# Kernel tuning notes

Measured on AMD Instinct MI355X. Metric: run time of the kernel, lower is better.

## Reference

```python
import jax, jax.numpy as jnp
import numpy as np

EPS = 1e-5  # BatchNorm1d default eps


def _proj_bn(x, W, gamma, beta, mean, var):
    # Conv1d(kernel=1, bias=False) == channel matmul, then inference BatchNorm1d.
    y = jnp.einsum('oc,bcn->bon', W, x)  # (B, C_out, N)
    scale = gamma / jnp.sqrt(var + EPS)  # (C_out,)
    shift = beta - mean * scale
    return y * scale[:, None] + shift[:, None]


def setup_inputs() -> dict:
    key = jax.random.key(0)
    ks = jax.random.split(key, 8)
    B, C, N = 8, 512, 2048
    inp = {
        'input': jax.random.normal(ks[0], (B, C, N), dtype=jnp.float32),
        'Wq': jax.random.normal(ks[1], (C, C), dtype=jnp.float32) * (1.0 / np.sqrt(C)),
        'gq': jnp.ones((C,), jnp.float32),
        'bq': jnp.zeros((C,), jnp.float32),
        'mq': jax.random.normal(ks[2], (C,), dtype=jnp.float32) * 0.1,
        'vq': jax.random.uniform(ks[3], (C,), dtype=jnp.float32) + 0.5,
        'Wk': jax.random.normal(ks[4], (C, C), dtype=jnp.float32) * (1.0 / np.sqrt(C)),
        'gk': jnp.ones((C,), jnp.float32),
        'bk': jnp.zeros((C,), jnp.float32),
        'mk': jax.random.normal(ks[5], (C,), dtype=jnp.float32) * 0.1,
        'vk': jax.random.uniform(ks[6], (C,), dtype=jnp.float32) + 0.5,
        'Wv': jax.random.normal(ks[7], (C, C), dtype=jnp.float32) * (1.0 / np.sqrt(C)),
        'gv': jnp.ones((C,), jnp.float32),
        'bv': jnp.zeros((C,), jnp.float32),
        'mv': jax.random.normal(jax.random.fold_in(key, 100), (C,), dtype=jnp.float32) * 0.1,
        'vv': jax.random.uniform(jax.random.fold_in(key, 101), (C,), dtype=jnp.float32) + 0.5,
    }
    return inp


def reference(input, Wq, gq, bq, mq, vq, Wk, gk, bk, mk, vk, Wv, gv, bv, mv, vv):
    q = _proj_bn(input, Wq, gq, bq, mq, vq)  # (B, C, N)
    k = _proj_bn(input, Wk, gk, bk, mk, vk)
    v = _proj_bn(input, Wv, gv, bv, mv, vv)
    # w[b, i, j] = sum_c q[b, c, i] * k[b, c, j]
    w = jnp.einsum('bci,bcj->bij', q, k)
    a = jax.nn.softmax(w, axis=-1)  # softmax over key axis j (dim 3 in torch)
    # c[b, c, i] = sum_j a[b, i, j] * v[b, c, j]  (== (v * w.softmax(3)).sum(3))
    return jnp.einsum('bij,bcj->bci', a, v)
```

## Files before the change

### kernel.cpp

```cpp
#include <hip/hip_runtime.h>
#include <cstdint>
#include <cstddef>

#define EPSV 1e-5f
constexpr int B_ = 8;
constexpr int C_ = 512;
constexpr int N_ = 2048;

typedef _Float16 f16x8 __attribute__((ext_vector_type(8)));
typedef float    f32x4 __attribute__((ext_vector_type(4)));

__device__ __forceinline__ unsigned short f16b(float f) {
    _Float16 h = (_Float16)f;
    return __builtin_bit_cast(unsigned short, h);
}

__device__ __forceinline__ void gload_lds16(const void* g, void* l) {
    __builtin_amdgcn_global_load_lds(
        (const __attribute__((address_space(1))) void*)g,
        (__attribute__((address_space(3))) void*)l, 16, 0, 0);
}

__global__ __launch_bounds__(256) void split_x_kernel(
    const float* __restrict__ x, unsigned short* __restrict__ xh)
{
    __shared__ float T[64][65];
    const int b = blockIdx.z, c0 = blockIdx.y * 64, n0 = blockIdx.x * 64;
    const float* xb = x + ((size_t)b * C_ + c0) * N_ + n0;
    const int tid = threadIdx.x;
    const int lr = tid >> 4;
    const int lcn = (tid & 15) * 4;
#pragma unroll
    for (int it = 0; it < 4; ++it) {
        float4 v = *(const float4*)&xb[(size_t)(lr + 16 * it) * N_ + lcn];
        T[lr + 16 * it][lcn + 0] = v.x;
        T[lr + 16 * it][lcn + 1] = v.y;
        T[lr + 16 * it][lcn + 2] = v.z;
        T[lr + 16 * it][lcn + 3] = v.w;
    }
    __syncthreads();
    const int n = tid >> 2, cb = (tid & 3) * 16;
    alignas(16) unsigned short h[16];
#pragma unroll
    for (int i = 0; i < 16; ++i)
        h[i] = f16b(T[cb + i][n]);
    const size_t o = ((size_t)b * N_ + n0 + n) * C_ + c0 + cb;
    *(uint4*)&xh[o]     = *(uint4*)&h[0];
    *(uint4*)&xh[o + 8] = *(uint4*)&h[8];
}

__global__ __launch_bounds__(256) void split_w_kernel(
    const float* __restrict__ W, unsigned short* __restrict__ wh)
{
    const int i = (blockIdx.x * 256 + threadIdx.x) * 4;
    float4 v = *(const float4*)&W[i];
    alignas(8) unsigned short h[4];
    h[0] = f16b(v.x); h[1] = f16b(v.y); h[2] = f16b(v.z); h[3] = f16b(v.w);
    *(ushort4*)&wh[i] = *(ushort4*)&h[0];
}

__global__ __launch_bounds__(512) void param_concat_kernel(
    const float* gq, const float* bq, const float* mq, const float* vq,
    const float* gk, const float* bk, const float* mk, const float* vk,
    const float* gv, const float* bv, const float* mv, const float* vv,
    float* sg, float* sb, float* sm, float* sv)
{
    const int i = threadIdx.x;
    sg[i] = gq[i];  sg[512 + i] = gk[i];  sg[1024 + i] = gv[i];
    sb[i] = bq[i];  sb[512 + i] = bk[i];  sb[1024 + i] = bv[i];
    sm[i] = mq[i];  sm[512 + i] = mk[i];  sm[1024 + i] = mv[i];
    sv[i] = vq[i];  sv[512 + i] = vk[i];  sv[1024 + i] = vv[i];
}

constexpr int EPI_QK = 0, EPI_PROJT = 2;

template <int EPI>
__global__ __launch_bounds__(512, 2) void qk256(
    const unsigned short* __restrict__ Ah, const unsigned short* __restrict__ Bh,
    int K, int lda, int ldb,
    long strideA, long strideB, long strideC, long strideC2,
    void* __restrict__ C0, void* __restrict__ C1, float* __restrict__ ML,
    const float* __restrict__ g, const float* __restrict__ bt,
    const float* __restrict__ mu, const float* __restrict__ var)
{
    __shared__ char smem[131072];

    const int id = blockIdx.x;
    const int bz = id & 7;
    const int s  = id >> 3;
    const int bx = s & 7, by = s >> 3;
    const int n0 = bx * 256;
    const int m0 = by * 256;

    const unsigned short* Ahb = Ah + (size_t)bz * strideA;
    const unsigned short* Bhb = Bh + (size_t)bz * strideB;

    const int tid  = threadIdx.x;
    const int lane = tid & 63;
    const int wv   = tid >> 6;
    const int wr   = wv >> 2, wc = wv & 3;
    const int WRB  = wr * 128, WCB = wc * 64;
    const int l4 = lane >> 4, l15 = lane & 15;

    const int srow  = tid >> 3;
    const int sslot = ((tid & 7) ^ (srow & 7)) * 8;

#define STAGE(t)                                                              \
    {                                                                         \
        char* dst = smem + ((t) & 1) * 65536;                                 \
        const unsigned short* asrc =                                          \
            Ahb + (size_t)(m0 + srow) * lda + (t) * 64 + sslot;               \
        _Pragma("unroll")                                                     \
        for (int u = 0; u < 4; ++u)                                           \
            gload_lds16(asrc + (size_t)(u * 64) * lda,                        \
                        dst + u * 8192 + tid * 16);                           \
        const unsigned short* bsrc =                                          \
            Bhb + (size_t)(n0 + srow) * ldb + (t) * 64 + sslot;               \
        _Pragma("unroll")                                                     \
        for (int u = 0; u < 4; ++u)                                           \
            gload_lds16(bsrc + (size_t)(u * 64) * ldb,                        \
                        dst + 32768 + u * 8192 + tid * 16);                   \
    }

    f32x4 acc[8][4] = {};
    const int NT = K / 64;

    STAGE(0);

    for (int t = 0; t < NT; ++t) {
        char* cur = smem + (t & 1) * 65536;
        __builtin_amdgcn_s_barrier();
        if (t + 1 < NT) {
            STAGE(t + 1);
            asm volatile("s_waitcnt vmcnt(8)" ::: "memory");
        } else {
            asm volatile("s_waitcnt vmcnt(0)" ::: "memory");
        }
        __builtin_amdgcn_s_barrier();

        f16x8 ah[8][2], bh[4][2];
#pragma unroll
        for (int m = 0; m < 8; ++m) {
            const int row = WRB + m * 16 + l15;
#pragma unroll
            for (int kk = 0; kk < 2; ++kk)
                ah[m][kk] = *(const f16x8*)(cur + row * 128 +
                                            (((kk << 2) | l4) ^ (row & 7)) * 16);
        }
#pragma unroll
        for (int n = 0; n < 4; ++n) {
            const int row = WCB + n * 16 + l15;
#pragma unroll
            for (int kk = 0; kk < 2; ++kk)
                bh[n][kk] = *(const f16x8*)(cur + 32768 + row * 128 +
                                            (((kk << 2) | l4) ^ (row & 7)) * 16);
        }
        __builtin_amdgcn_s_setprio(1);
#pragma unroll
        for (int kk = 0; kk < 2; ++kk)
#pragma unroll
            for (int m = 0; m < 8; ++m)
#pragma unroll
                for (int n = 0; n < 4; ++n)
                    acc[m][n] = __builtin_amdgcn_mfma_f32_16x16x32_f16(
                        ah[m][kk], bh[n][kk], acc[m][n], 0, 0, 0);
        __builtin_amdgcn_s_setprio(0);
    }
#undef STAGE

    if constexpr (EPI == EPI_QK) {
        unsigned short* H = (unsigned short*)C0 + (size_t)bz * strideC;
        const int tcol = bx * 4 + wc;
        const size_t mbase = (((size_t)bz * 32 + tcol) * 2) * 2048;
#pragma unroll
        for (int m = 0; m < 8; ++m) {
#pragma unroll
            for (int r = 0; r < 4; ++r) {
                float mx = fmaxf(fmaxf(acc[m][0][r], acc[m][1][r]),
                                 fmaxf(acc[m][2][r], acc[m][3][r]));
#pragma unroll
                for (int off = 1; off < 16; off <<= 1)
                    mx = fmaxf(mx, __shfl_xor(mx, off));
                float pe[4];
                float s2 = 0.f;
#pragma unroll
                for (int n = 0; n < 4; ++n) {
                    pe[n] = __expf(acc[m][n][r] - mx);
                    s2 += pe[n];
                }
#pragma unroll
                for (int off = 1; off < 16; off <<= 1)
                    s2 += __shfl_xor(s2, off);
                const int rloc = WRB + m * 16 + l4 * 4 + r;
                if (l15 == 0) {
                    ML[mbase + m0 + rloc] = mx;
                    ML[mbase + 2048 + m0 + rloc] = s2;
                }
#pragma unroll
                for (int n = 0; n < 4; ++n)
                    H[(size_t)(m0 + rloc) * 2048 + n0 + WCB + n * 16 + l15] =
                        f16b(pe[n]);
            }
        }
    } else {
        if (m0 < 1024) {
            unsigned short* H = (unsigned short*)C0 + (size_t)bz * strideC;
#pragma unroll
            for (int m = 0; m < 8; ++m) {
                const int mg = m0 + WRB + m * 16 + l4 * 4;
                float sc[4], sh[4];
#pragma unroll
                for (int r = 0; r < 4; ++r) {
                    const int o = mg + r;
                    sc[r] = g[o] * rsqrtf(var[o] + EPSV);
                    sh[r] = bt[o] - mu[o] * sc[r];
                }
#pragma unroll
                for (int n = 0; n < 4; ++n) {
                    const int ng = n0 + WCB + n * 16 + l15;
                    alignas(8) unsigned short h4[4];
#pragma unroll
                    for (int r = 0; r < 4; ++r)
                        h4[r] = f16b(acc[m][n][r] * sc[r] + sh[r]);
                    *(ushort4*)&H[(size_t)ng * 1024 + mg] = *(ushort4*)&h4[0];
                }
            }
        } else {
            unsigned short* V = (unsigned short*)C1 + (size_t)bz * strideC2;
#pragma unroll
            for (int m = 0; m < 8; ++m) {
                const int mg = m0 + WRB + m * 16 + l4 * 4;
                float sc[4], sh[4];
#pragma unroll
                for (int r = 0; r < 4; ++r) {
                    const int o = mg + r;
                    sc[r] = g[o] * rsqrtf(var[o] + EPSV);
                    sh[r] = bt[o] - mu[o] * sc[r];
                }
                const int d0 = mg - 1024;
#pragma unroll
                for (int n = 0; n < 4; ++n) {
                    const int ng = n0 + WCB + n * 16 + l15;
#pragma unroll
                    for (int r = 0; r < 4; ++r)
                        V[(size_t)(d0 + r) * 2048 + ng] =
                            f16b(acc[m][n][r] * sc[r] + sh[r]);
                }
            }
        }
    }
}

__global__ __launch_bounds__(512, 2) void pv256(
    const unsigned short* __restrict__ Ah, const unsigned short* __restrict__ Bh,
    int K, int lda, int ldb, long strideA, long strideB, long strideC,
    void* __restrict__ C0,
    const float* __restrict__ corr, const float* __restrict__ linv)
{
    constexpr int BUFSZ = 49152;
    __shared__ char smem[163840];

    const int id = blockIdx.x;
    const int bz = id & 7;
    const int s  = id >> 3;
    const int bx = s & 3, by = s >> 2;
    const int n0 = bx * 128;
    const int m0 = by * 256;

    const unsigned short* Ahb = Ah + (size_t)bz * strideA;
    const unsigned short* Bhb = Bh + (size_t)bz * strideB;

    const int tid  = threadIdx.x;
    const int lane = tid & 63;
    const int wv   = tid >> 6;
    const int wr   = wv >> 2, wc = wv & 3;
    const int WRB  = wr * 128, WCB = wc * 32;
    const int l4 = lane >> 4, l15 = lane & 15;

    const int srow = tid >> 3;
    const int sslot = ((tid & 7) ^ (srow & 7)) * 8;

    unsigned short* corrLds = (unsigned short*)(smem + 147456);
    for (int idx = tid; idx < 2048; idx += 512) {
        const int t = idx >> 6, i4 = (idx & 63) * 4;
        float4 c4 = *(const float4*)&corr[((size_t)bz * 32 + t) * 2048 + m0 + i4];
        alignas(8) unsigned short h4[4] =
            {f16b(c4.x), f16b(c4.y), f16b(c4.z), f16b(c4.w)};
        *(ushort4*)&corrLds[(size_t)t * 256 + i4] = *(ushort4*)&h4[0];
    }
    __syncthreads();

#define STAGE(t)                                                              \
    {                                                                         \
        char* dst = smem + ((t) % 3) * BUFSZ;                                 \
        const unsigned short* asrc =                                          \
            Ahb + (size_t)(m0 + srow) * lda + (t) * 64 + sslot;               \
        _Pragma("unroll")                                                     \
        for (int u = 0; u < 4; ++u)                                           \
            gload_lds16(asrc + (size_t)(u * 64) * lda,                        \
                        dst + u * 8192 + tid * 16);                           \
        const unsigned short* bsrc =                                          \
            Bhb + (size_t)(n0 + srow) * ldb + (t) * 64 + sslot;               \
        _Pragma("unroll")                                                     \
        for (int u = 0; u < 2; ++u)                                           \
            gload_lds16(bsrc + (size_t)(u * 64) * ldb,                        \
                        dst + 32768 + u * 8192 + tid * 16);                   \
    }

    f32x4 acc[8][2] = {};
    const int NT = K / 64;

    STAGE(0);
    STAGE(1);

    for (int t = 0; t < NT; ++t) {
        char* cur = smem + (t % 3) * BUFSZ;
        if (t + 2 < NT) {
            asm volatile("s_waitcnt vmcnt(6)" ::: "memory");
        } else {
            asm volatile("s_waitcnt vmcnt(0)" ::: "memory");
        }
        __builtin_amdgcn_s_barrier();
        asm volatile("" ::: "memory");
        if (t + 2 < NT) STAGE(t + 2);

        f16x8 ah[8][2], bh[2][2];
#pragma unroll
        for (int m = 0; m < 8; ++m) {
            const int row = WRB + m * 16 + l15;
#pragma unroll
            for (int kk = 0; kk < 2; ++kk)
                ah[m][kk] = *(const f16x8*)(cur + row * 128 +
                                            (((kk << 2) | l4) ^ (row & 7)) * 16);
        }
#pragma unroll
        for (int n = 0; n < 2; ++n) {
            const int row = WCB + n * 16 + l15;
#pragma unroll
            for (int kk = 0; kk < 2; ++kk)
                bh[n][kk] = *(const f16x8*)(cur + 32768 + row * 128 +
                                            (((kk << 2) | l4) ^ (row & 7)) * 16);
        }
#pragma unroll
        for (int m = 0; m < 8; ++m) {
            const _Float16 cf = ((const _Float16*)corrLds)
                [(size_t)t * 256 + WRB + m * 16 + l15];
            ah[m][0] = ah[m][0] * cf;
            ah[m][1] = ah[m][1] * cf;
        }
        __builtin_amdgcn_s_setprio(1);
#pragma unroll
        for (int kk = 0; kk < 2; ++kk)
#pragma unroll
            for (int m = 0; m < 8; ++m)
#pragma unroll
                for (int n = 0; n < 2; ++n)
                    acc[m][n] = __builtin_amdgcn_mfma_f32_16x16x32_f16(
                        ah[m][kk], bh[n][kk], acc[m][n], 0, 0, 0);
        __builtin_amdgcn_s_setprio(0);
    }
#undef STAGE

    float* Cb = (float*)C0 + (size_t)bz * strideC;
    const float* lb = linv + (size_t)bz * 2048;
#pragma unroll
    for (int m = 0; m < 8; ++m) {
        const int mrow = m0 + WRB + m * 16 + l4 * 4;
        float lv[4];
#pragma unroll
        for (int r = 0; r < 4; ++r)
            lv[r] = lb[mrow + r];
#pragma unroll
        for (int n = 0; n < 2; ++n) {
            const int col = n0 + WCB + n * 16 + l15;
            float4 o4 = make_float4(acc[m][n][0] * lv[0],
                                    acc[m][n][1] * lv[1],
                                    acc[m][n][2] * lv[2],
                                    acc[m][n][3] * lv[3]);
            *(float4*)&Cb[(size_t)col * 2048 + mrow] = o4;
        }
    }
}

__global__ __launch_bounds__(256) void ml_combine_kernel(
    const float* __restrict__ ml, float* __restrict__ corr,
    float* __restrict__ linv)
{
    const int idx = blockIdx.x * 256 + threadIdx.x;
    const int b = idx >> 11, i = idx & 2047;
    const float* base = ml + ((size_t)b * 32) * 2 * 2048 + i;
    float M = -3.0e38f;
#pragma unroll 8
    for (int t = 0; t < 32; ++t)
        M = fmaxf(M, base[(size_t)t * 4096]);
    float L = 0.f;
    float* cb = corr + (size_t)b * 32 * 2048 + i;
#pragma unroll 8
    for (int t = 0; t < 32; ++t) {
        const float c = __expf(base[(size_t)t * 4096] - M);
        L += c * base[(size_t)t * 4096 + 2048];
        cb[(size_t)t * 2048] = c;
    }
    linv[idx] = 1.0f / L;
}

extern "C" void kernel_launch(void* const* d_in, const int* in_sizes, int n_in,
                              void* d_out, int out_size, void* d_ws, size_t ws_size,
                              hipStream_t stream)
{
    (void)in_sizes; (void)n_in; (void)out_size; (void)ws_size;
    const float* x  = (const float*)d_in[0];
    const float* Wq = (const float*)d_in[1];
    const float* gq = (const float*)d_in[2];
    const float* bq = (const float*)d_in[3];
    const float* mq = (const float*)d_in[4];
    const float* vq = (const float*)d_in[5];
    const float* Wk = (const float*)d_in[6];
    const float* gk = (const float*)d_in[7];
    const float* bk = (const float*)d_in[8];
    const float* mk = (const float*)d_in[9];
    const float* vk = (const float*)d_in[10];
    const float* Wv = (const float*)d_in[11];
    const float* gv = (const float*)d_in[12];
    const float* bv = (const float*)d_in[13];
    const float* mv = (const float*)d_in[14];
    const float* vv = (const float*)d_in[15];
    float* out = (float*)d_out;

    const size_t MiB = 1048576;
    char* ws = (char*)d_ws;
    unsigned short* Wst = (unsigned short*)(ws);
    unsigned short* Wqh = Wst;
    unsigned short* Wkh = Wst + 512 * 512;
    unsigned short* Wvh = Wst + 1024 * 512;
    unsigned short* vbf  = (unsigned short*)(ws + 2 * MiB);
    unsigned short* qkTh = (unsigned short*)(ws + 18 * MiB);
    unsigned short* xTh  = (unsigned short*)(ws + 50 * MiB);
    unsigned short* pbuf = (unsigned short*)(ws + 66 * MiB);
    float* mlbuf = (float*)(ws + 130 * MiB);
    float* corr  = (float*)(ws + 134 * MiB);
    float* linv  = (float*)(ws + 136 * MiB);
    float* sg = (float*)(ws + 136 * MiB + 65536);
    float* sb = sg + 1536;
    float* sm = sb + 1536;
    float* sv = sm + 1536;

    const long BS = (long)N_ * C_;
    const long QKS = (long)N_ * 1024;

    split_x_kernel<<<dim3(N_ / 64, C_ / 64, B_), 256, 0, stream>>>(x, xTh);
    split_w_kernel<<<dim3(256), 256, 0, stream>>>(Wq, Wqh);
    split_w_kernel<<<dim3(256), 256, 0, stream>>>(Wk, Wkh);
    split_w_kernel<<<dim3(256), 256, 0, stream>>>(Wv, Wvh);
    param_concat_kernel<<<dim3(1), 512, 0, stream>>>(
        gq, bq, mq, vq, gk, bk, mk, vk, gv, bv, mv, vv, sg, sb, sm, sv);

    qk256<EPI_PROJT><<<dim3(384), 512, 0, stream>>>(
        Wst, xTh, 512, 512, 512, 0, BS, QKS, BS, qkTh, vbf,
        nullptr, sg, sb, sm, sv);

    qk256<EPI_QK><<<dim3(512), 512, 0, stream>>>(
        qkTh, qkTh + 512, 512, 1024, 1024, QKS, QKS, (long)N_ * N_, 0,
        pbuf, nullptr, mlbuf, nullptr, nullptr, nullptr, nullptr);

    ml_combine_kernel<<<dim3(B_ * N_ / 256), 256, 0, stream>>>(
        mlbuf, corr, linv);

    pv256<<<dim3(256), 512, 0, stream>>>(
        pbuf, vbf, 2048, 2048, 2048, (long)N_ * N_, BS, BS, out, corr, linv);
}
```

Measured before the change: 176.9 us.

## Retile qk256 GEMM to 256x128 tiles with K-step 32 and higher occupancy

Shrinks the qk256 output tile from 256x256 to 256x128 and the K step from 64 to 32. Waves become a 4x2 grid with 4x4 accumulators, LDS drops to 48KB, and the staging and swizzle are redone for 64-byte rows. Launch bounds ask for 4 blocks per CU and the grids double, aiming for more resident blocks and better latency hiding. The cost is lower data reuse per block, more barriers per unit of K, and tight register limits that may force spills.

```diff
diff --git a/kernel.cpp b/kernel.cpp
--- a/kernel.cpp
+++ b/kernel.cpp
@@ -75,7 +75,7 @@
 constexpr int EPI_QK = 0, EPI_PROJT = 2;
 
 template <int EPI>
-__global__ __launch_bounds__(512, 2) void qk256(
+__global__ __launch_bounds__(512, 4) void qk256(
     const unsigned short* __restrict__ Ah, const unsigned short* __restrict__ Bh,
     int K, int lda, int ldb,
     long strideA, long strideB, long strideC, long strideC2,
@@ -83,13 +83,13 @@
     const float* __restrict__ g, const float* __restrict__ bt,
     const float* __restrict__ mu, const float* __restrict__ var)
 {
-    __shared__ char smem[131072];
+    __shared__ char smem[49152];
 
     const int id = blockIdx.x;
     const int bz = id & 7;
     const int s  = id >> 3;
-    const int bx = s & 7, by = s >> 3;
-    const int n0 = bx * 256;
+    const int bx = s & 15, by = s >> 4;
+    const int n0 = bx * 128;
     const int m0 = by * 256;
 
     const unsigned short* Ahb = Ah + (size_t)bz * strideA;
@@ -98,82 +98,75 @@
     const int tid  = threadIdx.x;
     const int lane = tid & 63;
     const int wv   = tid >> 6;
-    const int wr   = wv >> 2, wc = wv & 3;
-    const int WRB  = wr * 128, WCB = wc * 64;
+    const int wr   = wv >> 1, wc = wv & 1;
+    const int WRB  = wr * 64, WCB = wc * 64;
     const int l4 = lane >> 4, l15 = lane & 15;
-
-    const int srow  = tid >> 3;
-    const int sslot = ((tid & 7) ^ (srow & 7)) * 8;
 
 #define STAGE(t)                                                              \
     {                                                                         \
-        char* dst = smem + ((t) & 1) * 65536;                                 \
-        const unsigned short* asrc =                                          \
-            Ahb + (size_t)(m0 + srow) * lda + (t) * 64 + sslot;               \
+        char* dst = smem + ((t) & 1) * 24576;                                 \
         _Pragma("unroll")                                                     \
-        for (int u = 0; u < 4; ++u)                                           \
-            gload_lds16(asrc + (size_t)(u * 64) * lda,                        \
-                        dst + u * 8192 + tid * 16);                           \
-        const unsigned short* bsrc =                                          \
-            Bhb + (size_t)(n0 + srow) * ldb + (t) * 64 + sslot;               \
-        _Pragma("unroll")                                                     \
-        for (int u = 0; u < 4; ++u)                                           \
-            gload_lds16(bsrc + (size_t)(u * 64) * ldb,                        \
-                        dst + 32768 + u * 8192 + tid * 16);                   \
-    }
-
-    f32x4 acc[8][4] = {};
-    const int NT = K / 64;
+        for (int u = 0; u < 2; ++u) {                                         \
+            const int L = u * 512 + tid;                                      \
+            const int row = L >> 2;                                           \
+            const int ssl = ((L & 3) ^ ((row >> 1) & 3)) * 8;                 \
+            gload_lds16(Ahb + (size_t)(m0 + row) * lda + (t) * 32 + ssl,      \
+                        dst + L * 16);                                        \
+        }                                                                     \
+        {                                                                     \
+            const int row = tid >> 2;                                         \
+            const int ssl = ((tid & 3) ^ ((row >> 1) & 3)) * 8;               \
+            gload_lds16(Bhb + (size_t)(n0 + row) * ldb + (t) * 32 + ssl,      \
+                        dst + 16384 + tid * 16);                              \
+        }                                                                     \
+    }
+
+    f32x4 acc[4][4] = {};
+    const int NT = K / 32;
 
     STAGE(0);
 
     for (int t = 0; t < NT; ++t) {
-        char* cur = smem + (t & 1) * 65536;
+        char* cur = smem + (t & 1) * 24576;
         __builtin_amdgcn_s_barrier();
         if (t + 1 < NT) {
             STAGE(t + 1);
-            asm volatile("s_waitcnt vmcnt(8)" ::: "memory");
+            asm volatile("s_waitcnt vmcnt(3)" ::: "memory");
         } else {
             asm volatile("s_waitcnt vmcnt(0)" ::: "memory");
         }
         __builtin_amdgcn_s_barrier();
 
-        f16x8 ah[8][2], bh[4][2];
-#pragma unroll
-        for (int m = 0; m < 8; ++m) {
+        f16x8 ah[4], bh[4];
+#pragma unroll
+        for (int m = 0; m < 4; ++m) {
             const int row = WRB + m * 16 + l15;
-#pragma unroll
-            for (int kk = 0; kk < 2; ++kk)
-                ah[m][kk] = *(const f16x8*)(cur + row * 128 +
-                                            (((kk << 2) | l4) ^ (row & 7)) * 16);
+            ah[m] = *(const f16x8*)(cur + row * 64 +
+                                    ((l4 ^ ((row >> 1) & 3)) * 16));
         }
 #pragma unroll
         for (int n = 0; n < 4; ++n) {
             const int row = WCB + n * 16 + l15;
-#pragma unroll
-            for (int kk = 0; kk < 2; ++kk)
-                bh[n][kk] = *(const f16x8*)(cur + 32768 + row * 128 +
-                                            (((kk << 2) | l4) ^ (row & 7)) * 16);
+            bh[n] = *(const f16x8*)(cur + 16384 + row * 64 +
+                                    ((l4 ^ ((row >> 1) & 3)) * 16));
         }
         __builtin_amdgcn_s_setprio(1);
 #pragma unroll
-        for (int kk = 0; kk < 2; ++kk)
-#pragma unroll
-            for (int m = 0; m < 8; ++m)
-#pragma unroll
-                for (int n = 0; n < 4; ++n)
-                    acc[m][n] = __builtin_amdgcn_mfma_f32_16x16x32_f16(
-                        ah[m][kk], bh[n][kk], acc[m][n], 0, 0, 0);
+        for (int m = 0; m < 4; ++m)
+#pragma unroll
+            for (int n = 0; n < 4; ++n)
+                acc[m][n] = __builtin_amdgcn_mfma_f32_16x16x32_f16(
+                    ah[m], bh[n], acc[m][n], 0, 0, 0);
         __builtin_amdgcn_s_setprio(0);
     }
 #undef STAGE
 
     if constexpr (EPI == EPI_QK) {
         unsigned short* H = (unsigned short*)C0 + (size_t)bz * strideC;
-        const int tcol = bx * 4 + wc;
+        const int tcol = bx * 2 + wc;
         const size_t mbase = (((size_t)bz * 32 + tcol) * 2) * 2048;
 #pragma unroll
-        for (int m = 0; m < 8; ++m) {
+        for (int m = 0; m < 4; ++m) {
 #pragma unroll
             for (int r = 0; r < 4; ++r) {
                 float mx = fmaxf(fmaxf(acc[m][0][r], acc[m][1][r]),
@@ -206,7 +199,7 @@
         if (m0 < 1024) {
             unsigned short* H = (unsigned short*)C0 + (size_t)bz * strideC;
 #pragma unroll
-            for (int m = 0; m < 8; ++m) {
+            for (int m = 0; m < 4; ++m) {
                 const int mg = m0 + WRB + m * 16 + l4 * 4;
                 float sc[4], sh[4];
 #pragma unroll
@@ -228,7 +221,7 @@
         } else {
             unsigned short* V = (unsigned short*)C1 + (size_t)bz * strideC2;
 #pragma unroll
-            for (int m = 0; m < 8; ++m) {
+            for (int m = 0; m < 4; ++m) {
                 const int mg = m0 + WRB + m * 16 + l4 * 4;
                 float sc[4], sh[4];
 #pragma unroll
@@ -455,11 +448,11 @@
     param_concat_kernel<<<dim3(1), 512, 0, stream>>>(
         gq, bq, mq, vq, gk, bk, mk, vk, gv, bv, mv, vv, sg, sb, sm, sv);
 
-    qk256<EPI_PROJT><<<dim3(384), 512, 0, stream>>>(
+    qk256<EPI_PROJT><<<dim3(768), 512, 0, stream>>>(
         Wst, xTh, 512, 512, 512, 0, BS, QKS, BS, qkTh, vbf,
         nullptr, sg, sb, sm, sv);
 
-    qk256<EPI_QK><<<dim3(512), 512, 0, stream>>>(
+    qk256<EPI_QK><<<dim3(1024), 512, 0, stream>>>(
         qkTh, qkTh + 512, 512, 1024, 1024, QKS, QKS, (long)N_ * N_, 0,
         pbuf, nullptr, mlbuf, nullptr, nullptr, nullptr, nullptr);
 
```

New measurement: 169.4 us. 4.3% less time.
